# Kernel tuning notes

Measured on AMD Instinct MI355X. Metric: run time of the kernel, lower is better.

The kernel has to match this reference:

```python
import jax, jax.numpy as jnp
import numpy as np

B, N, M = 32, 65536, 64
IMG = 640.0
POS_THR, NEG_THR = 0.5, 0.4
ALPHA, GAMMA = 0.25, 2.0
BBOX_W = 2.0
EPS = 1e-6


def setup_inputs() -> dict:
    key = jax.random.key(0)
    k1, k2, k3, k4, k5 = jax.random.split(key, 5)
    # predictions: cx, cy in [0, IMG], w, h in [8, 72], obj logit ~ N(0,1)
    cxcy = jax.random.uniform(k1, (B, N, 2), jnp.float32) * IMG
    wh = jax.random.uniform(k2, (B, N, 2), jnp.float32) * 64.0 + 8.0
    obj = jax.random.normal(k3, (B, N, 1), jnp.float32)
    predictions = jnp.concatenate([cxcy, wh, obj], axis=-1)  # [B, N, 5]
    # ground-truth boxes in xyxy, centers in [0, IMG], sizes in [10, 100]
    gcxcy = jax.random.uniform(k4, (B, M, 2), jnp.float32) * IMG
    gwh = jax.random.uniform(k5, (B, M, 2), jnp.float32) * 90.0 + 10.0
    gt_boxes = jnp.concatenate([gcxcy - gwh / 2, gcxcy + gwh / 2], axis=-1)  # [B, M, 4]
    return {"predictions": predictions, "gt_boxes": gt_boxes}


def _focal(logits, targets):
    # stable BCE-with-logits, then focal modulation
    bce = jnp.maximum(logits, 0.0) - logits * targets + jnp.log1p(jnp.exp(-jnp.abs(logits)))
    p = jax.nn.sigmoid(logits)
    p_t = jnp.where(targets == 1.0, p, 1.0 - p)
    alpha_t = jnp.where(targets == 1.0, ALPHA, 1.0 - ALPHA)
    return alpha_t * (1.0 - p_t) ** GAMMA * bce


def _pairwise_iou(pb, gb):
    # pb: [N,4] xyxy, gb: [M,4] xyxy -> [N,M]
    x1 = jnp.maximum(pb[:, None, 0], gb[None, :, 0])
    y1 = jnp.maximum(pb[:, None, 1], gb[None, :, 1])
    x2 = jnp.minimum(pb[:, None, 2], gb[None, :, 2])
    y2 = jnp.minimum(pb[:, None, 3], gb[None, :, 3])
    inter = jnp.clip(x2 - x1, 0.0) * jnp.clip(y2 - y1, 0.0)
    area_p = (pb[:, 2] - pb[:, 0]) * (pb[:, 3] - pb[:, 1])
    area_g = (gb[:, 2] - gb[:, 0]) * (gb[:, 3] - gb[:, 1])
    union = area_p[:, None] + area_g[None, :] - inter
    return inter / jnp.clip(union, EPS)


def _giou_term(pb, gb):
    # elementwise 1 - GIoU; pb, gb: [N,4]
    x1 = jnp.maximum(pb[:, 0], gb[:, 0]); y1 = jnp.maximum(pb[:, 1], gb[:, 1])
    x2 = jnp.minimum(pb[:, 2], gb[:, 2]); y2 = jnp.minimum(pb[:, 3], gb[:, 3])
    inter = jnp.clip(x2 - x1, 0.0) * jnp.clip(y2 - y1, 0.0)
    area_p = (pb[:, 2] - pb[:, 0]) * (pb[:, 3] - pb[:, 1])
    area_g = (gb[:, 2] - gb[:, 0]) * (gb[:, 3] - gb[:, 1])
    union = area_p + area_g - inter
    iou = inter / jnp.clip(union, EPS)
    ex1 = jnp.minimum(pb[:, 0], gb[:, 0]); ey1 = jnp.minimum(pb[:, 1], gb[:, 1])
    ex2 = jnp.maximum(pb[:, 2], gb[:, 2]); ey2 = jnp.maximum(pb[:, 3], gb[:, 3])
    enc = (ex2 - ex1) * (ey2 - ey1)
    giou = iou - (enc - union) / jnp.clip(enc, EPS)
    return 1.0 - giou


def _per_image(pred, gt):
    # pred: [N,5] (cx,cy,w,h,obj), gt: [M,4] xyxy
    cx, cy, w, h = pred[:, 0], pred[:, 1], pred[:, 2], pred[:, 3]
    pb = jnp.stack([cx - w / 2, cy - h / 2, cx + w / 2, cy + h / 2], axis=1)  # decode to xyxy
    obj = pred[:, 4]
    ious = _pairwise_iou(pb, gt)  # [N, M]
    best_pred_per_gt = ious.max(axis=0)              # [M]
    best_pred_idx = jnp.argmax(ious, axis=0)         # [M]
    best_gt_per_pred = ious.max(axis=1)              # [N]
    best_gt_idx = jnp.argmax(ious, axis=1)           # [N]
    # force-match each GT's best anchor if its IoU > 0.1 (scatter-max)
    pos_scatter = jnp.zeros((pred.shape[0],), jnp.int32).at[best_pred_idx].max(
        (best_pred_per_gt > 0.1).astype(jnp.int32))
    pos = (pos_scatter > 0) | (best_gt_per_pred > POS_THR)
    neg = best_gt_per_pred < NEG_THR
    valid = pos | neg
    t = pos.astype(jnp.float32)
    fl = _focal(obj, t)
    vcnt = valid.sum().astype(jnp.float32)
    cls_loss = jnp.where(vcnt > 0, (fl * valid).sum() / jnp.maximum(vcnt, 1.0), 0.0)
    matched = gt[best_gt_idx]                        # [N,4]
    gterm = _giou_term(pb, matched)                  # [N]
    pcnt = pos.sum().astype(jnp.float32)
    reg_loss = jnp.where(pcnt > 0, (gterm * pos).sum() / jnp.maximum(pcnt, 1.0), 0.0)
    return cls_loss, reg_loss, pos.sum()


def reference(predictions, gt_boxes):
    cls_b, reg_b, npos_b = jax.vmap(_per_image)(predictions, gt_boxes)
    num_pos = jnp.maximum(npos_b.sum(), 1).astype(jnp.float32)
    bsz = jnp.float32(predictions.shape[0])
    total_cls = cls_b.sum() / bsz
    total_reg = reg_b.sum() / num_pos * bsz
    return total_cls + BBOX_W * total_reg
```

## Files before the change

kernel.cpp:

```cpp
#include <hip/hip_runtime.h>

#define NB 32
#define NPRED 65536
#define NGT 64
#define BLK 256
#define SLICES 64
#define PPT 4
#define NCB 128
#define CBIN_SCALE 0.2f

#define POS_THR 0.5f
#define NEG_THR 0.4f
#define SCAT_THR 0.1f
#define EPSF 1e-6f


__device__ __forceinline__ int cbin(float x) {
    int bi = (int)(x * CBIN_SCALE);
    return max(0, min(NCB - 1, bi));
}

__device__ __forceinline__ float focal_shared(float l, bool pos) {
    float e  = expf(-fabsf(l));
    float lg = log1pf(e);
    float rp = 1.f / (1.f + e);
    float p  = (l >= 0.f) ? rp : (1.f - rp);
    if (pos) { float q = 1.f - p; return 0.25f * q * q * ((fmaxf(l, 0.f) - l) + lg); }
    return 0.75f * p * p * (fmaxf(l, 0.f) + lg);
}

__device__ __forceinline__ float giou_term(float px1, float py1, float px2, float py2,
                                           float gx1, float gy1, float gx2, float gy2) {
    float x1 = fmaxf(px1, gx1), y1 = fmaxf(py1, gy1);
    float x2 = fminf(px2, gx2), y2 = fminf(py2, gy2);
    float dx = fmaxf(__fsub_rn(x2, x1), 0.f);
    float dy = fmaxf(__fsub_rn(y2, y1), 0.f);
    float inter = __fmul_rn(dx, dy);
    float ap = __fmul_rn(__fsub_rn(px2, px1), __fsub_rn(py2, py1));
    float ag = __fmul_rn(__fsub_rn(gx2, gx1), __fsub_rn(gy2, gy1));
    float uni = __fsub_rn(__fadd_rn(ap, ag), inter);
    float iou = __fdiv_rn(inter, fmaxf(uni, EPSF));
    float ex1 = fminf(px1, gx1), ey1 = fminf(py1, gy1);
    float ex2 = fmaxf(px2, gx2), ey2 = fmaxf(py2, gy2);
    float enc = __fmul_rn(__fsub_rn(ex2, ex1), __fsub_rn(ey2, ey1));
    float giou = __fsub_rn(iou, __fdiv_rn(__fsub_rn(enc, uni), fmaxf(enc, EPSF)));
    return __fsub_rn(1.f, giou);
}


__global__ __launch_bounds__(BLK) void passA(
    const float* __restrict__ pred, const float* __restrict__ gt,
    unsigned long long* __restrict__ keysP,
    float4* __restrict__ partS,
    unsigned* __restrict__ done)
{
    const int b = blockIdx.y;
    const int slice = blockIdx.x;
    const int tid = threadIdx.x;
    const int lane = tid & 63;
    const int wv = tid >> 6;

    if (b == 0 && slice == 0 && tid == 0) *done = 0u;

    __shared__ float sgx1[NGT + 1], sgy1[NGT + 1], sgx2[NGT + 1], sgy2[NGT + 1], sgar[NGT + 1];
    __shared__ unsigned long long skey[NGT];
    __shared__ unsigned long long cums[4][NCB];
    __shared__ float rfl[BLK / 64], rgt[BLK / 64];
    __shared__ int rvp[BLK / 64];

    const unsigned base_n = (unsigned)(slice * (BLK * PPT));
    const float4* src4 = (const float4*)(pred + (size_t)b * NPRED * 5 + (size_t)base_n * 5)
                         + (size_t)tid * 5;
    float4 q0 = src4[0], q1 = src4[1], q2 = src4[2], q3 = src4[3], q4 = src4[4];

    const float4* gtb = (const float4*)(gt + (size_t)b * NGT * 4);
    float4 gmine;
    if (tid < NGT) gmine = gtb[tid];
    ((unsigned long long*)cums)[tid] = 0ULL;
    ((unsigned long long*)cums)[tid + BLK] = 0ULL;
    if (tid < NGT) {
        sgx1[tid] = gmine.x; sgy1[tid] = gmine.y;
        sgx2[tid] = gmine.z; sgy2[tid] = gmine.w;
        sgar[tid] = __fmul_rn(__fsub_rn(gmine.z, gmine.x), __fsub_rn(gmine.w, gmine.y));
        skey[tid] = 0ULL;
    } else if (tid == NGT) {
        sgx1[NGT] = 0.f; sgy1[NGT] = 0.f; sgx2[NGT] = 0.f; sgy2[NGT] = 0.f; sgar[NGT] = 0.f;
    }
    __syncthreads();

    if (tid < NGT) {
        unsigned long long bit = 1ULL << tid;
        atomicOr(&cums[0][cbin(gmine.x)], bit);
        atomicOr(&cums[1][cbin(gmine.z)], bit);
        atomicOr(&cums[2][cbin(gmine.y)], bit);
        atomicOr(&cums[3][cbin(gmine.w)], bit);
    }
    __syncthreads();

    {
        unsigned long long v0 = cums[wv][2 * lane];
        unsigned long long v1 = cums[wv][2 * lane + 1];
        unsigned long long v = v0 | v1;
        if ((wv & 1) == 0) {
            #pragma unroll
            for (int off = 1; off < 64; off <<= 1) {
                unsigned long long t = __shfl_up(v, off);
                if (lane >= off) v |= t;
            }
            unsigned long long prev = __shfl_up(v, 1);
            if (lane == 0) prev = 0ULL;
            cums[wv][2 * lane]     = prev | v0;
            cums[wv][2 * lane + 1] = v;
        } else {
            #pragma unroll
            for (int off = 1; off < 64; off <<= 1) {
                unsigned long long t = __shfl_down(v, off);
                if (lane + off < 64) v |= t;
            }
            unsigned long long nxt = __shfl_down(v, 1);
            if (lane == 63) nxt = 0ULL;
            cums[wv][2 * lane]     = v;
            cums[wv][2 * lane + 1] = v1 | nxt;
        }
    }
    __syncthreads();

    const float cxa[PPT] = {q0.x, q1.y, q2.z, q3.w};
    const float cya[PPT] = {q0.y, q1.z, q2.w, q4.x};
    const float wa [PPT] = {q0.z, q1.w, q3.x, q4.y};
    const float ha [PPT] = {q0.w, q2.x, q3.y, q4.z};
    const float oba[PPT] = {q1.x, q2.y, q3.z, q4.w};

    float acc_fl = 0.f, acc_gt = 0.f;
    int acc_vp = 0;

    #pragma unroll
    for (int i = 0; i < PPT; ++i) {
        const float px1 = __fsub_rn(cxa[i], __fmul_rn(wa[i], 0.5f));
        const float py1 = __fsub_rn(cya[i], __fmul_rn(ha[i], 0.5f));
        const float px2 = __fadd_rn(cxa[i], __fmul_rn(wa[i], 0.5f));
        const float py2 = __fadd_rn(cya[i], __fmul_rn(ha[i], 0.5f));
        const float area_p = __fmul_rn(__fsub_rn(px2, px1), __fsub_rn(py2, py1));

        unsigned long long m = (cums[1][cbin(px1)] & cums[0][cbin(px2)])
                             & (cums[3][cbin(py1)] & cums[2][cbin(py2)]);

        const unsigned n = base_n + (unsigned)(PPT * tid + i);
        const unsigned long long nkey = (unsigned long long)(~n);

        float best_iou = 0.f;
        int best_j = 0;

        int j0 = NGT, j1 = NGT;
        if (m) { j0 = __ffsll(m) - 1; m &= m - 1; }
        if (m) { j1 = __ffsll(m) - 1; m &= m - 1; }
        {
            float ax1 = sgx1[j0], ay1 = sgy1[j0], ax2 = sgx2[j0], ay2 = sgy2[j0], aga = sgar[j0];
            float bx1 = sgx1[j1], by1 = sgy1[j1], bx2 = sgx2[j1], by2 = sgy2[j1], agb = sgar[j1];
            float x1 = fmaxf(px1, ax1), y1 = fmaxf(py1, ay1);
            float x2 = fminf(px2, ax2), y2 = fminf(py2, ay2);
            float dx = fmaxf(__fsub_rn(x2, x1), 0.f);
            float dy = fmaxf(__fsub_rn(y2, y1), 0.f);
            float inter = __fmul_rn(dx, dy);
            float uni = __fsub_rn(__fadd_rn(area_p, aga), inter);
            float iou = __fdiv_rn(inter, fmaxf(uni, EPSF));
            iou = (inter > 0.f) ? iou : 0.f;
            if (iou > best_iou) { best_iou = iou; best_j = j0; }
            if (iou > SCAT_THR)
                atomicMax(&skey[j0], (((unsigned long long)__float_as_uint(iou)) << 32) | nkey);

            float X1 = fmaxf(px1, bx1), Y1 = fmaxf(py1, by1);
            float X2 = fminf(px2, bx2), Y2 = fminf(py2, by2);
            float dX = fmaxf(__fsub_rn(X2, X1), 0.f);
            float dY = fmaxf(__fsub_rn(Y2, Y1), 0.f);
            float interB = __fmul_rn(dX, dY);
            float uniB = __fsub_rn(__fadd_rn(area_p, agb), interB);
            float iouB = __fdiv_rn(interB, fmaxf(uniB, EPSF));
            iouB = (interB > 0.f) ? iouB : 0.f;
            if (iouB > best_iou) { best_iou = iouB; best_j = j1; }
            if (iouB > SCAT_THR)
                atomicMax(&skey[j1], (((unsigned long long)__float_as_uint(iouB)) << 32) | nkey);
        }

        while (m) {
            int ja = __ffsll(m) - 1; m &= m - 1;
            int jb = -1;
            if (m) { jb = __ffsll(m) - 1; m &= m - 1; }
            int jbc = (jb >= 0) ? jb : NGT;
            float ax1 = sgx1[ja], ay1 = sgy1[ja], ax2 = sgx2[ja], ay2 = sgy2[ja], aga = sgar[ja];
            float bx1 = sgx1[jbc], by1 = sgy1[jbc], bx2 = sgx2[jbc], by2 = sgy2[jbc], agb = sgar[jbc];
            {
                float x1 = fmaxf(px1, ax1), y1 = fmaxf(py1, ay1);
                float x2 = fminf(px2, ax2), y2 = fminf(py2, ay2);
                float dx = fmaxf(__fsub_rn(x2, x1), 0.f);
                float dy = fmaxf(__fsub_rn(y2, y1), 0.f);
                float inter = __fmul_rn(dx, dy);
                if (inter > 0.f) {
                    float uni = __fsub_rn(__fadd_rn(area_p, aga), inter);
                    float iou = __fdiv_rn(inter, fmaxf(uni, EPSF));
                    if (iou > best_iou) { best_iou = iou; best_j = ja; }
                    if (iou > SCAT_THR)
                        atomicMax(&skey[ja], (((unsigned long long)__float_as_uint(iou)) << 32) | nkey);
                }
            }
            if (jb >= 0) {
                float x1 = fmaxf(px1, bx1), y1 = fmaxf(py1, by1);
                float x2 = fminf(px2, bx2), y2 = fminf(py2, by2);
                float dx = fmaxf(__fsub_rn(x2, x1), 0.f);
                float dy = fmaxf(__fsub_rn(y2, y1), 0.f);
                float inter = __fmul_rn(dx, dy);
                if (inter > 0.f) {
                    float uni = __fsub_rn(__fadd_rn(area_p, agb), inter);
                    float iou = __fdiv_rn(inter, fmaxf(uni, EPSF));
                    if (iou > best_iou) { best_iou = iou; best_j = jb; }
                    if (iou > SCAT_THR)
                        atomicMax(&skey[jb], (((unsigned long long)__float_as_uint(iou)) << 32) | nkey);
                }
            }
        }

        const bool pos0   = best_iou > POS_THR;
        const bool negf   = best_iou < NEG_THR;
        const bool valid0 = pos0 || negf;
        if (valid0) acc_fl += focal_shared(oba[i], pos0);
        if (pos0) {
            acc_gt += giou_term(px1, py1, px2, py2,
                                sgx1[best_j], sgy1[best_j], sgx2[best_j], sgy2[best_j]);
        }
        acc_vp += (valid0 ? 1 : 0) | (pos0 ? 0x10000 : 0);
    }

    for (int off = 32; off; off >>= 1) {
        acc_fl += __shfl_down(acc_fl, off);
        acc_gt += __shfl_down(acc_gt, off);
        acc_vp += __shfl_down(acc_vp, off);
    }
    if (lane == 0) { rfl[wv] = acc_fl; rgt[wv] = acc_gt; rvp[wv] = acc_vp; }
    __syncthreads();
    if (tid == 0) {
        float sfl = 0.f, sgt2 = 0.f; int svp = 0;
        #pragma unroll
        for (int i = 0; i < BLK / 64; ++i) { sfl += rfl[i]; sgt2 += rgt[i]; svp += rvp[i]; }
        partS[b * SLICES + slice] = make_float4(sfl, sgt2, __int_as_float(svp), 0.f);
    }
    if (tid < NGT) {
        keysP[((size_t)b * SLICES + slice) * NGT + tid] = skey[tid];
    }
}


__global__ __launch_bounds__(64) void passB(
    const float* __restrict__ pred, const float* __restrict__ gt,
    const unsigned long long* __restrict__ keysP,
    const float4* __restrict__ partS,
    float* __restrict__ cls_b, float* __restrict__ reg_b, int* __restrict__ npos_b,
    unsigned* __restrict__ done, float* __restrict__ out)
{
    const int b = blockIdx.x;
    const int lane = threadIdx.x;

    __shared__ float4 sgt[NGT];
    __shared__ unsigned cn_list[NGT];

    const float4* gtb = (const float4*)(gt + (size_t)b * NGT * 4);
    float4 gj = gtb[lane];
    sgt[lane] = gj;

    const unsigned long long* kp = keysP + (size_t)b * SLICES * NGT + lane;
    unsigned long long key = 0ULL;
    #pragma unroll 16
    for (int s = 0; s < SLICES; ++s) {
        unsigned long long k = kp[(size_t)s * NGT];
        key = (k > key) ? k : key;
    }

    float miou = __uint_as_float((unsigned)(key >> 32));
    unsigned n = ~((unsigned)(key & 0xFFFFFFFFULL));
    bool qual = miou > SCAT_THR;

    bool unique = qual;
    for (int j2 = 0; j2 < NGT; ++j2) {
        unsigned bn = __shfl(n, j2);
        int bq = __shfl((int)qual, j2);
        if (bq && j2 < lane && bn == n) unique = false;
    }
    unsigned long long mask = __ballot(unique ? 1 : 0);
    int NC = __popcll(mask);
    int slot = __popcll(mask & ((1ULL << lane) - 1ULL));
    if (unique) cn_list[slot] = n;
    __syncthreads();

    float cx = 0.f, cy = 0.f, w = 0.f, h = 0.f, obj = 0.f;
    if (lane < NC) {
        const float* p = pred + (size_t)b * NPRED * 5 + (size_t)cn_list[lane] * 5;
        cx = p[0]; cy = p[1]; w = p[2]; h = p[3]; obj = p[4];
    }
    float px1 = __fsub_rn(cx, __fmul_rn(w, 0.5f));
    float py1 = __fsub_rn(cy, __fmul_rn(h, 0.5f));
    float px2 = __fadd_rn(cx, __fmul_rn(w, 0.5f));
    float py2 = __fadd_rn(cy, __fmul_rn(h, 0.5f));
    float area_p = __fmul_rn(__fsub_rn(px2, px1), __fsub_rn(py2, py1));

    float bv = 0.f; int bj = 0;
    #pragma unroll 4
    for (int j = 0; j < NGT; ++j) {
        float4 g = sgt[j];
        float x1 = fmaxf(px1, g.x), y1 = fmaxf(py1, g.y);
        float x2 = fminf(px2, g.z), y2 = fminf(py2, g.w);
        float dx = fmaxf(__fsub_rn(x2, x1), 0.f);
        float dy = fmaxf(__fsub_rn(y2, y1), 0.f);
        float inter = __fmul_rn(dx, dy);
        if (inter > 0.f) {
            float ag = __fmul_rn(__fsub_rn(g.z, g.x), __fsub_rn(g.w, g.y));
            float uni = __fsub_rn(__fadd_rn(area_p, ag), inter);
            float iou = __fdiv_rn(inter, fmaxf(uni, EPSF));
            if (iou > bv) { bv = iou; bj = j; }
        }
    }

    double add_fl = 0.0, add_gt = 0.0;
    int add_v = 0, add_p = 0;
    if (lane < NC && !(bv > POS_THR)) {
        bool was_neg = bv < NEG_THR;
        float f1 = focal_shared(obj, true);
        float f0 = focal_shared(obj, false);
        add_fl = (double)f1 - (was_neg ? (double)f0 : 0.0);
        add_v = was_neg ? 0 : 1;
        add_p = 1;
        float4 gb = sgt[bj];
        add_gt = (double)giou_term(px1, py1, px2, py2, gb.x, gb.y, gb.z, gb.w);
    }

    float4 ps = partS[b * SLICES + lane];
    double sfl = (double)ps.x + add_fl;
    double sgt2 = (double)ps.y + add_gt;
    int vpk = __float_as_int(ps.z);
    int sv = (vpk & 0xFFFF) + add_v;
    int sp = (vpk >> 16) + add_p;

    for (int off = 32; off; off >>= 1) {
        sfl  += __shfl_down(sfl, off);
        sgt2 += __shfl_down(sgt2, off);
        sv   += __shfl_down(sv, off);
        sp   += __shfl_down(sp, off);
    }

    if (lane == 0) {
        cls_b[b] = (sv > 0) ? (float)(sfl / (double)(sv > 1 ? sv : 1)) : 0.f;
        reg_b[b] = (sp > 0) ? (float)(sgt2 / (double)(sp > 1 ? sp : 1)) : 0.f;
        npos_b[b] = sp;
    }

    __threadfence();
    unsigned t = 0;
    if (lane == 0) t = atomicAdd(done, 1u);
    t = __shfl(t, 0);
    if (t == NB - 1) {
        __threadfence();
        volatile float* vc = cls_b;
        volatile float* vr = reg_b;
        volatile int*   vn = npos_b;
        float cv = (lane < NB) ? vc[lane] : 0.f;
        float rv = (lane < NB) ? vr[lane] : 0.f;
        int   nv = (lane < NB) ? vn[lane] : 0;
        for (int off = 32; off; off >>= 1) {
            cv += __shfl_down(cv, off);
            rv += __shfl_down(rv, off);
            nv += __shfl_down(nv, off);
        }
        if (lane == 0) {
            float num_pos = fmaxf((float)nv, 1.f);
            out[0] = cv / (float)NB + 2.0f * (rv / num_pos * (float)NB);
        }
    }
}


extern "C" void kernel_launch(void* const* d_in, const int* in_sizes, int n_in,
                              void* d_out, int out_size, void* d_ws, size_t ws_size,
                              hipStream_t stream) {
    const float* pred = (const float*)d_in[0];
    const float* gt   = (const float*)d_in[1];
    float* out = (float*)d_out;

    char* ws = (char*)d_ws;
    unsigned long long* keysP = (unsigned long long*)(ws + 0);
    float4* partS = (float4*)(ws + (size_t)NB * SLICES * NGT * 8);
    char* tail = ws + (size_t)NB * SLICES * NGT * 8 + (size_t)NB * SLICES * 16;
    float* cls_b   = (float*)(tail);
    float* reg_b   = (float*)(tail + 128);
    int* npos_b    = (int*)(tail + 256);
    unsigned* done = (unsigned*)(tail + 384);

    dim3 gridA(SLICES, NB);
    passA<<<gridA, BLK, 0, stream>>>(pred, gt, keysP, partS, done);
    passB<<<NB, 64, 0, stream>>>(pred, gt, keysP, partS,
                                 cls_b, reg_b, npos_b, done, out);
}
```

Before: 114.4 us.

## Fuse per-image finalize pass into main kernel via last-block-done counters

Folds the second kernel into the first. Each block increments a per-image counter, and the last slice block for an image does that image's key reduction, force-match fixup and partial-sum reduction. A second global counter then lets the last image's tail block compute the final scalar. This removes one kernel launch and the serialization gap between passes. In exchange it adds a hipMemsetAsync to reset the counters, which is itself another stream operation, plus extra fences and atomics in every block.

```diff
diff --git a/kernel.cpp b/kernel.cpp
--- a/kernel.cpp
+++ b/kernel.cpp
@@ -52,7 +52,9 @@
     const float* __restrict__ pred, const float* __restrict__ gt,
     unsigned long long* __restrict__ keysP,
     float4* __restrict__ partS,
-    unsigned* __restrict__ done)
+    float* __restrict__ cls_b, float* __restrict__ reg_b, int* __restrict__ npos_b,
+    unsigned* __restrict__ doneB, unsigned* __restrict__ done2,
+    float* __restrict__ out)
 {
     const int b = blockIdx.y;
     const int slice = blockIdx.x;
@@ -60,13 +62,14 @@
     const int lane = tid & 63;
     const int wv = tid >> 6;
 
-    if (b == 0 && slice == 0 && tid == 0) *done = 0u;
-
     __shared__ float sgx1[NGT + 1], sgy1[NGT + 1], sgx2[NGT + 1], sgy2[NGT + 1], sgar[NGT + 1];
     __shared__ unsigned long long skey[NGT];
     __shared__ unsigned long long cums[4][NCB];
     __shared__ float rfl[BLK / 64], rgt[BLK / 64];
     __shared__ int rvp[BLK / 64];
+    __shared__ int isTail;
+    __shared__ float4 tgt[NGT];
+    __shared__ unsigned tcn[NGT];
 
     const unsigned base_n = (unsigned)(slice * (BLK * PPT));
     const float4* src4 = (const float4*)(pred + (size_t)b * NPRED * 5 + (size_t)base_n * 5)
@@ -246,131 +249,126 @@
     if (tid < NGT) {
         keysP[((size_t)b * SLICES + slice) * NGT + tid] = skey[tid];
     }
-}
-
-
-__global__ __launch_bounds__(64) void passB(
-    const float* __restrict__ pred, const float* __restrict__ gt,
-    const unsigned long long* __restrict__ keysP,
-    const float4* __restrict__ partS,
-    float* __restrict__ cls_b, float* __restrict__ reg_b, int* __restrict__ npos_b,
-    unsigned* __restrict__ done, float* __restrict__ out)
-{
-    const int b = blockIdx.x;
-    const int lane = threadIdx.x;
-
-    __shared__ float4 sgt[NGT];
-    __shared__ unsigned cn_list[NGT];
-
-    const float4* gtb = (const float4*)(gt + (size_t)b * NGT * 4);
-    float4 gj = gtb[lane];
-    sgt[lane] = gj;
-
-    const unsigned long long* kp = keysP + (size_t)b * SLICES * NGT + lane;
-    unsigned long long key = 0ULL;
-    #pragma unroll 16
-    for (int s = 0; s < SLICES; ++s) {
-        unsigned long long k = kp[(size_t)s * NGT];
-        key = (k > key) ? k : key;
-    }
-
-    float miou = __uint_as_float((unsigned)(key >> 32));
-    unsigned n = ~((unsigned)(key & 0xFFFFFFFFULL));
-    bool qual = miou > SCAT_THR;
-
-    bool unique = qual;
-    for (int j2 = 0; j2 < NGT; ++j2) {
-        unsigned bn = __shfl(n, j2);
-        int bq = __shfl((int)qual, j2);
-        if (bq && j2 < lane && bn == n) unique = false;
-    }
-    unsigned long long mask = __ballot(unique ? 1 : 0);
-    int NC = __popcll(mask);
-    int slot = __popcll(mask & ((1ULL << lane) - 1ULL));
-    if (unique) cn_list[slot] = n;
-    __syncthreads();
-
-    float cx = 0.f, cy = 0.f, w = 0.f, h = 0.f, obj = 0.f;
-    if (lane < NC) {
-        const float* p = pred + (size_t)b * NPRED * 5 + (size_t)cn_list[lane] * 5;
-        cx = p[0]; cy = p[1]; w = p[2]; h = p[3]; obj = p[4];
-    }
-    float px1 = __fsub_rn(cx, __fmul_rn(w, 0.5f));
-    float py1 = __fsub_rn(cy, __fmul_rn(h, 0.5f));
-    float px2 = __fadd_rn(cx, __fmul_rn(w, 0.5f));
-    float py2 = __fadd_rn(cy, __fmul_rn(h, 0.5f));
-    float area_p = __fmul_rn(__fsub_rn(px2, px1), __fsub_rn(py2, py1));
-
-    float bv = 0.f; int bj = 0;
-    #pragma unroll 4
-    for (int j = 0; j < NGT; ++j) {
-        float4 g = sgt[j];
-        float x1 = fmaxf(px1, g.x), y1 = fmaxf(py1, g.y);
-        float x2 = fminf(px2, g.z), y2 = fminf(py2, g.w);
-        float dx = fmaxf(__fsub_rn(x2, x1), 0.f);
-        float dy = fmaxf(__fsub_rn(y2, y1), 0.f);
-        float inter = __fmul_rn(dx, dy);
-        if (inter > 0.f) {
-            float ag = __fmul_rn(__fsub_rn(g.z, g.x), __fsub_rn(g.w, g.y));
-            float uni = __fsub_rn(__fadd_rn(area_p, ag), inter);
-            float iou = __fdiv_rn(inter, fmaxf(uni, EPSF));
-            if (iou > bv) { bv = iou; bj = j; }
-        }
-    }
-
-    double add_fl = 0.0, add_gt = 0.0;
-    int add_v = 0, add_p = 0;
-    if (lane < NC && !(bv > POS_THR)) {
-        bool was_neg = bv < NEG_THR;
-        float f1 = focal_shared(obj, true);
-        float f0 = focal_shared(obj, false);
-        add_fl = (double)f1 - (was_neg ? (double)f0 : 0.0);
-        add_v = was_neg ? 0 : 1;
-        add_p = 1;
-        float4 gb = sgt[bj];
-        add_gt = (double)giou_term(px1, py1, px2, py2, gb.x, gb.y, gb.z, gb.w);
-    }
-
-    float4 ps = partS[b * SLICES + lane];
-    double sfl = (double)ps.x + add_fl;
-    double sgt2 = (double)ps.y + add_gt;
-    int vpk = __float_as_int(ps.z);
-    int sv = (vpk & 0xFFFF) + add_v;
-    int sp = (vpk >> 16) + add_p;
-
-    for (int off = 32; off; off >>= 1) {
-        sfl  += __shfl_down(sfl, off);
-        sgt2 += __shfl_down(sgt2, off);
-        sv   += __shfl_down(sv, off);
-        sp   += __shfl_down(sp, off);
-    }
-
-    if (lane == 0) {
-        cls_b[b] = (sv > 0) ? (float)(sfl / (double)(sv > 1 ? sv : 1)) : 0.f;
-        reg_b[b] = (sp > 0) ? (float)(sgt2 / (double)(sp > 1 ? sp : 1)) : 0.f;
-        npos_b[b] = sp;
-    }
 
     __threadfence();
-    unsigned t = 0;
-    if (lane == 0) t = atomicAdd(done, 1u);
-    t = __shfl(t, 0);
-    if (t == NB - 1) {
+    __syncthreads();
+    if (tid == 0) {
+        unsigned old = atomicAdd(&doneB[b], 1u);
+        isTail = (old == SLICES - 1) ? 1 : 0;
+    }
+    __syncthreads();
+    if (!isTail) return;
+
+    __threadfence();
+    if (tid < 64) {
+        float4 gj = gtb[lane];
+        tgt[lane] = gj;
+
+        const unsigned long long* kp = keysP + (size_t)b * SLICES * NGT + lane;
+        unsigned long long key = 0ULL;
+        #pragma unroll 16
+        for (int s = 0; s < SLICES; ++s) {
+            unsigned long long k = kp[(size_t)s * NGT];
+            key = (k > key) ? k : key;
+        }
+
+        float miou = __uint_as_float((unsigned)(key >> 32));
+        unsigned n = ~((unsigned)(key & 0xFFFFFFFFULL));
+        bool qual = miou > SCAT_THR;
+
+        bool unique = qual;
+        for (int j2 = 0; j2 < NGT; ++j2) {
+            unsigned bn = __shfl(n, j2);
+            int bq = __shfl((int)qual, j2);
+            if (bq && j2 < lane && bn == n) unique = false;
+        }
+        unsigned long long mask = __ballot(unique ? 1 : 0);
+        int NC = __popcll(mask);
+        int slot = __popcll(mask & ((1ULL << lane) - 1ULL));
+        if (unique) tcn[slot] = n;
+
+        float cx = 0.f, cy = 0.f, w = 0.f, h = 0.f, obj = 0.f;
+        if (lane < NC) {
+            const float* p = pred + (size_t)b * NPRED * 5 + (size_t)tcn[lane] * 5;
+            cx = p[0]; cy = p[1]; w = p[2]; h = p[3]; obj = p[4];
+        }
+        float px1 = __fsub_rn(cx, __fmul_rn(w, 0.5f));
+        float py1 = __fsub_rn(cy, __fmul_rn(h, 0.5f));
+        float px2 = __fadd_rn(cx, __fmul_rn(w, 0.5f));
+        float py2 = __fadd_rn(cy, __fmul_rn(h, 0.5f));
+        float area_p = __fmul_rn(__fsub_rn(px2, px1), __fsub_rn(py2, py1));
+
+        float bv = 0.f; int bj = 0;
+        #pragma unroll 4
+        for (int j = 0; j < NGT; ++j) {
+            float4 g = tgt[j];
+            float x1 = fmaxf(px1, g.x), y1 = fmaxf(py1, g.y);
+            float x2 = fminf(px2, g.z), y2 = fminf(py2, g.w);
+            float dx = fmaxf(__fsub_rn(x2, x1), 0.f);
+            float dy = fmaxf(__fsub_rn(y2, y1), 0.f);
+            float inter = __fmul_rn(dx, dy);
+            if (inter > 0.f) {
+                float ag = __fmul_rn(__fsub_rn(g.z, g.x), __fsub_rn(g.w, g.y));
+                float uni = __fsub_rn(__fadd_rn(area_p, ag), inter);
+                float iou = __fdiv_rn(inter, fmaxf(uni, EPSF));
+                if (iou > bv) { bv = iou; bj = j; }
+            }
+        }
+
+        double add_fl = 0.0, add_gt = 0.0;
+        int add_v = 0, add_p = 0;
+        if (lane < NC && !(bv > POS_THR)) {
+            bool was_neg = bv < NEG_THR;
+            float f1 = focal_shared(obj, true);
+            float f0 = focal_shared(obj, false);
+            add_fl = (double)f1 - (was_neg ? (double)f0 : 0.0);
+            add_v = was_neg ? 0 : 1;
+            add_p = 1;
+            float4 gb = tgt[bj];
+            add_gt = (double)giou_term(px1, py1, px2, py2, gb.x, gb.y, gb.z, gb.w);
+        }
+
+        float4 ps = partS[b * SLICES + lane];
+        double sfl = (double)ps.x + add_fl;
+        double sgt2 = (double)ps.y + add_gt;
+        int vpk = __float_as_int(ps.z);
+        int sv = (vpk & 0xFFFF) + add_v;
+        int sp = (vpk >> 16) + add_p;
+
+        for (int off = 32; off; off >>= 1) {
+            sfl  += __shfl_down(sfl, off);
+            sgt2 += __shfl_down(sgt2, off);
+            sv   += __shfl_down(sv, off);
+            sp   += __shfl_down(sp, off);
+        }
+
+        if (lane == 0) {
+            cls_b[b] = (sv > 0) ? (float)(sfl / (double)(sv > 1 ? sv : 1)) : 0.f;
+            reg_b[b] = (sp > 0) ? (float)(sgt2 / (double)(sp > 1 ? sp : 1)) : 0.f;
+            npos_b[b] = sp;
+        }
+
         __threadfence();
-        volatile float* vc = cls_b;
-        volatile float* vr = reg_b;
-        volatile int*   vn = npos_b;
-        float cv = (lane < NB) ? vc[lane] : 0.f;
-        float rv = (lane < NB) ? vr[lane] : 0.f;
-        int   nv = (lane < NB) ? vn[lane] : 0;
-        for (int off = 32; off; off >>= 1) {
-            cv += __shfl_down(cv, off);
-            rv += __shfl_down(rv, off);
-            nv += __shfl_down(nv, off);
-        }
-        if (lane == 0) {
-            float num_pos = fmaxf((float)nv, 1.f);
-            out[0] = cv / (float)NB + 2.0f * (rv / num_pos * (float)NB);
+        unsigned t = 0;
+        if (lane == 0) t = atomicAdd(done2, 1u);
+        t = __shfl(t, 0);
+        if (t == NB - 1) {
+            __threadfence();
+            volatile float* vc = cls_b;
+            volatile float* vr = reg_b;
+            volatile int*   vn = npos_b;
+            float cv = (lane < NB) ? vc[lane] : 0.f;
+            float rv = (lane < NB) ? vr[lane] : 0.f;
+            int   nv = (lane < NB) ? vn[lane] : 0;
+            for (int off = 32; off; off >>= 1) {
+                cv += __shfl_down(cv, off);
+                rv += __shfl_down(rv, off);
+                nv += __shfl_down(nv, off);
+            }
+            if (lane == 0) {
+                float num_pos = fmaxf((float)nv, 1.f);
+                out[0] = cv / (float)NB + 2.0f * (rv / num_pos * (float)NB);
+            }
         }
     }
 }
@@ -390,10 +388,12 @@
     float* cls_b   = (float*)(tail);
     float* reg_b   = (float*)(tail + 128);
     int* npos_b    = (int*)(tail + 256);
-    unsigned* done = (unsigned*)(tail + 384);
+    unsigned* doneB = (unsigned*)(tail + 384);
+    unsigned* done2 = (unsigned*)(tail + 512);
+
+    hipMemsetAsync(tail + 384, 0, 256, stream);
 
     dim3 gridA(SLICES, NB);
-    passA<<<gridA, BLK, 0, stream>>>(pred, gt, keysP, partS, done);
-    passB<<<NB, 64, 0, stream>>>(pred, gt, keysP, partS,
-                                 cls_b, reg_b, npos_b, done, out);
-}
+    passA<<<gridA, BLK, 0, stream>>>(pred, gt, keysP, partS,
+                                     cls_b, reg_b, npos_b, doneB, done2, out);
+}
```

Result: slower. 235.6 us (+105.9%).

## Issue prediction loads via inline asm early and pack GT boxes as float4 in LDS

Applied to the files above, without the earlier changes.

Prediction and GT loads are issued with inline asm at kernel start. Only the GT load is waited on before the shared-memory bin setup, so the prediction loads stay in flight during the setup and its barriers. GT boxes move from five separate scalar LDS arrays into one float4 array plus an area array, so each candidate lookup becomes one 128-bit LDS read instead of four scalar reads. The risk is that the inline asm waitcnt depends on load issue order, and the sched barriers stop the compiler from reordering around them.

```diff
diff --git a/kernel.cpp b/kernel.cpp
--- a/kernel.cpp
+++ b/kernel.cpp
@@ -13,6 +13,8 @@
 #define NEG_THR 0.4f
 #define SCAT_THR 0.1f
 #define EPSF 1e-6f
+
+typedef float f32x4 __attribute__((ext_vector_type(4)));
 
 
 __device__ __forceinline__ int cbin(float x) {
@@ -62,38 +64,46 @@
 
     if (b == 0 && slice == 0 && tid == 0) *done = 0u;
 
-    __shared__ float sgx1[NGT + 1], sgy1[NGT + 1], sgx2[NGT + 1], sgy2[NGT + 1], sgar[NGT + 1];
+    __shared__ float4 sgbox[NGT + 1];
+    __shared__ float sgar[NGT + 1];
     __shared__ unsigned long long skey[NGT];
     __shared__ unsigned long long cums[4][NCB];
     __shared__ float rfl[BLK / 64], rgt[BLK / 64];
     __shared__ int rvp[BLK / 64];
 
     const unsigned base_n = (unsigned)(slice * (BLK * PPT));
-    const float4* src4 = (const float4*)(pred + (size_t)b * NPRED * 5 + (size_t)base_n * 5)
-                         + (size_t)tid * 5;
-    float4 q0 = src4[0], q1 = src4[1], q2 = src4[2], q3 = src4[3], q4 = src4[4];
-
     const float4* gtb = (const float4*)(gt + (size_t)b * NGT * 4);
-    float4 gmine;
-    if (tid < NGT) gmine = gtb[tid];
+    const float* gaddr = (const float*)(gtb + (tid & 63));
+    const float* paddr = (const float*)((const float4*)(pred + (size_t)b * NPRED * 5
+                                        + (size_t)base_n * 5) + (size_t)tid * 5);
+    f32x4 gq, q0, q1, q2, q3, q4;
+    asm volatile("global_load_dwordx4 %0, %1, off"           : "=v"(gq) : "v"(gaddr));
+    asm volatile("global_load_dwordx4 %0, %1, off"           : "=v"(q0) : "v"(paddr));
+    asm volatile("global_load_dwordx4 %0, %1, off offset:16" : "=v"(q1) : "v"(paddr));
+    asm volatile("global_load_dwordx4 %0, %1, off offset:32" : "=v"(q2) : "v"(paddr));
+    asm volatile("global_load_dwordx4 %0, %1, off offset:48" : "=v"(q3) : "v"(paddr));
+    asm volatile("global_load_dwordx4 %0, %1, off offset:64" : "=v"(q4) : "v"(paddr));
+    asm volatile("s_waitcnt vmcnt(5)" ::: "memory");
+    __builtin_amdgcn_sched_barrier(0);
+
     ((unsigned long long*)cums)[tid] = 0ULL;
     ((unsigned long long*)cums)[tid + BLK] = 0ULL;
     if (tid < NGT) {
-        sgx1[tid] = gmine.x; sgy1[tid] = gmine.y;
-        sgx2[tid] = gmine.z; sgy2[tid] = gmine.w;
-        sgar[tid] = __fmul_rn(__fsub_rn(gmine.z, gmine.x), __fsub_rn(gmine.w, gmine.y));
+        sgbox[tid] = make_float4(gq[0], gq[1], gq[2], gq[3]);
+        sgar[tid] = __fmul_rn(__fsub_rn(gq[2], gq[0]), __fsub_rn(gq[3], gq[1]));
         skey[tid] = 0ULL;
     } else if (tid == NGT) {
-        sgx1[NGT] = 0.f; sgy1[NGT] = 0.f; sgx2[NGT] = 0.f; sgy2[NGT] = 0.f; sgar[NGT] = 0.f;
+        sgbox[NGT] = make_float4(0.f, 0.f, 0.f, 0.f);
+        sgar[NGT] = 0.f;
     }
     __syncthreads();
 
     if (tid < NGT) {
         unsigned long long bit = 1ULL << tid;
-        atomicOr(&cums[0][cbin(gmine.x)], bit);
-        atomicOr(&cums[1][cbin(gmine.z)], bit);
-        atomicOr(&cums[2][cbin(gmine.y)], bit);
-        atomicOr(&cums[3][cbin(gmine.w)], bit);
+        atomicOr(&cums[0][cbin(gq[0])], bit);
+        atomicOr(&cums[1][cbin(gq[2])], bit);
+        atomicOr(&cums[2][cbin(gq[1])], bit);
+        atomicOr(&cums[3][cbin(gq[3])], bit);
     }
     __syncthreads();
 
@@ -125,11 +135,14 @@
     }
     __syncthreads();
 
-    const float cxa[PPT] = {q0.x, q1.y, q2.z, q3.w};
-    const float cya[PPT] = {q0.y, q1.z, q2.w, q4.x};
-    const float wa [PPT] = {q0.z, q1.w, q3.x, q4.y};
-    const float ha [PPT] = {q0.w, q2.x, q3.y, q4.z};
-    const float oba[PPT] = {q1.x, q2.y, q3.z, q4.w};
+    asm volatile("s_waitcnt vmcnt(0)" ::: "memory");
+    __builtin_amdgcn_sched_barrier(0);
+
+    const float cxa[PPT] = {q0[0], q1[1], q2[2], q3[3]};
+    const float cya[PPT] = {q0[1], q1[2], q2[3], q4[0]};
+    const float wa [PPT] = {q0[2], q1[3], q3[0], q4[1]};
+    const float ha [PPT] = {q0[3], q2[0], q3[1], q4[2]};
+    const float oba[PPT] = {q1[0], q2[1], q3[2], q4[3]};
 
     float acc_fl = 0.f, acc_gt = 0.f;
     int acc_vp = 0;
@@ -155,10 +168,10 @@
         if (m) { j0 = __ffsll(m) - 1; m &= m - 1; }
         if (m) { j1 = __ffsll(m) - 1; m &= m - 1; }
         {
-            float ax1 = sgx1[j0], ay1 = sgy1[j0], ax2 = sgx2[j0], ay2 = sgy2[j0], aga = sgar[j0];
-            float bx1 = sgx1[j1], by1 = sgy1[j1], bx2 = sgx2[j1], by2 = sgy2[j1], agb = sgar[j1];
-            float x1 = fmaxf(px1, ax1), y1 = fmaxf(py1, ay1);
-            float x2 = fminf(px2, ax2), y2 = fminf(py2, ay2);
+            float4 ga = sgbox[j0]; float aga = sgar[j0];
+            float4 gbx = sgbox[j1]; float agb = sgar[j1];
+            float x1 = fmaxf(px1, ga.x), y1 = fmaxf(py1, ga.y);
+            float x2 = fminf(px2, ga.z), y2 = fminf(py2, ga.w);
             float dx = fmaxf(__fsub_rn(x2, x1), 0.f);
             float dy = fmaxf(__fsub_rn(y2, y1), 0.f);
             float inter = __fmul_rn(dx, dy);
@@ -169,8 +182,8 @@
             if (iou > SCAT_THR)
                 atomicMax(&skey[j0], (((unsigned long long)__float_as_uint(iou)) << 32) | nkey);
 
-            float X1 = fmaxf(px1, bx1), Y1 = fmaxf(py1, by1);
-            float X2 = fminf(px2, bx2), Y2 = fminf(py2, by2);
+            float X1 = fmaxf(px1, gbx.x), Y1 = fmaxf(py1, gbx.y);
+            float X2 = fminf(px2, gbx.z), Y2 = fminf(py2, gbx.w);
             float dX = fmaxf(__fsub_rn(X2, X1), 0.f);
             float dY = fmaxf(__fsub_rn(Y2, Y1), 0.f);
             float interB = __fmul_rn(dX, dY);
@@ -187,11 +200,11 @@
             int jb = -1;
             if (m) { jb = __ffsll(m) - 1; m &= m - 1; }
             int jbc = (jb >= 0) ? jb : NGT;
-            float ax1 = sgx1[ja], ay1 = sgy1[ja], ax2 = sgx2[ja], ay2 = sgy2[ja], aga = sgar[ja];
-            float bx1 = sgx1[jbc], by1 = sgy1[jbc], bx2 = sgx2[jbc], by2 = sgy2[jbc], agb = sgar[jbc];
+            float4 ga = sgbox[ja]; float aga = sgar[ja];
+            float4 gbx = sgbox[jbc]; float agb = sgar[jbc];
             {
-                float x1 = fmaxf(px1, ax1), y1 = fmaxf(py1, ay1);
-                float x2 = fminf(px2, ax2), y2 = fminf(py2, ay2);
+                float x1 = fmaxf(px1, ga.x), y1 = fmaxf(py1, ga.y);
+                float x2 = fminf(px2, ga.z), y2 = fminf(py2, ga.w);
                 float dx = fmaxf(__fsub_rn(x2, x1), 0.f);
                 float dy = fmaxf(__fsub_rn(y2, y1), 0.f);
                 float inter = __fmul_rn(dx, dy);
@@ -204,8 +217,8 @@
                 }
             }
             if (jb >= 0) {
-                float x1 = fmaxf(px1, bx1), y1 = fmaxf(py1, by1);
-                float x2 = fminf(px2, bx2), y2 = fminf(py2, by2);
+                float x1 = fmaxf(px1, gbx.x), y1 = fmaxf(py1, gbx.y);
+                float x2 = fminf(px2, gbx.z), y2 = fminf(py2, gbx.w);
                 float dx = fmaxf(__fsub_rn(x2, x1), 0.f);
                 float dy = fmaxf(__fsub_rn(y2, y1), 0.f);
                 float inter = __fmul_rn(dx, dy);
@@ -224,8 +237,8 @@
         const bool valid0 = pos0 || negf;
         if (valid0) acc_fl += focal_shared(oba[i], pos0);
         if (pos0) {
-            acc_gt += giou_term(px1, py1, px2, py2,
-                                sgx1[best_j], sgy1[best_j], sgx2[best_j], sgy2[best_j]);
+            float4 gbb = sgbox[best_j];
+            acc_gt += giou_term(px1, py1, px2, py2, gbb.x, gbb.y, gbb.z, gbb.w);
         }
         acc_vp += (valid0 ? 1 : 0) | (pos0 ? 0x10000 : 0);
     }
```

After: 113.5 us. No clear change (-0.8%).
